# Kernel tuning notes

Measured on AMD Instinct MI355X. Metric: run time of the kernel, lower is better.

## Reference

```python
import jax, jax.numpy as jnp
import numpy as np

N_QUBITS = 8
DEPTH = 3


def _apply_1q(state, U, q):
    # state: (2,)*n complex, apply 2x2 unitary U on qubit axis q
    state = jnp.moveaxis(state, q, -1)
    state = state @ U.T
    return jnp.moveaxis(state, -1, q)


def _ry(state, theta, q):
    h = theta * 0.5
    c, s = jnp.cos(h), jnp.sin(h)
    U = jnp.stack([jnp.stack([c, -s]), jnp.stack([s, c])]).astype(jnp.complex64)
    return _apply_1q(state, U, q)


def _rz(state, theta, q):
    h = theta * 0.5
    d = jnp.stack([jnp.exp(-1j * h), jnp.exp(1j * h)]).astype(jnp.complex64)
    state = jnp.moveaxis(state, q, -1) * d
    return jnp.moveaxis(state, -1, q)


def _cx(state, c, t):
    # CNOT with control c, target t: flip target amplitudes where control=1
    state = jnp.moveaxis(state, (c, t), (-2, -1))
    s0 = state[..., 0, :]
    s1 = state[..., 1, ::-1]
    state = jnp.stack([s0, s1], axis=-2)
    return jnp.moveaxis(state, (-2, -1), (c, t))


def _simulate(angles, qparams):
    # Single-sample circuit: RY angle encoding, then DEPTH layers of (RZ,RY) per
    # qubit + CX ring. Returns <Z_0> (Hamiltonian 'Z' + 'I'*(n-1)).
    state = jnp.zeros((2,) * N_QUBITS, jnp.complex64).at[(0,) * N_QUBITS].set(1.0)
    for q in range(N_QUBITS):
        state = _ry(state, angles[q], q)
    idx = 0
    for _ in range(DEPTH):
        for q in range(N_QUBITS):
            state = _rz(state, qparams[idx], q); idx += 1
            state = _ry(state, qparams[idx], q); idx += 1
        for i in range(N_QUBITS):
            state = _cx(state, i, (i + 1) % N_QUBITS)
    probs = jnp.abs(state) ** 2
    return probs[0].sum() - probs[1].sum()


def setup_inputs() -> dict:
    key = jax.random.key(0)
    ks = jax.random.split(key, 6)
    B, F, H = 16384, 16, 256
    nq = 2 * N_QUBITS * DEPTH  # 48 variational params
    return {
        "x": jax.random.normal(ks[0], (B, F), jnp.float32),
        "enc_w1": jax.random.normal(ks[1], (H, F), jnp.float32) / np.sqrt(F).astype(np.float32),
        "enc_b1": jnp.zeros((H,), jnp.float32),
        "enc_w2": jax.random.normal(ks[2], (N_QUBITS, H), jnp.float32) / np.sqrt(H).astype(np.float32),
        "enc_b2": jnp.zeros((N_QUBITS,), jnp.float32),
        "qparams": jax.random.normal(ks[3], (nq,), jnp.float32) * 0.1,
        "dec_w1": jax.random.normal(ks[4], (H, 1), jnp.float32),
        "dec_b1": jnp.zeros((H,), jnp.float32),
        "dec_w2": jax.random.normal(ks[5], (1, H), jnp.float32) / np.sqrt(H).astype(np.float32),
        "dec_b2": jnp.zeros((1,), jnp.float32),
    }


def reference(x, enc_w1, enc_b1, enc_w2, enc_b2, qparams, dec_w1, dec_b1, dec_w2, dec_b2):
    # encoder: Linear -> ReLU -> Linear -> Tanh, scaled by pi (angle encoding)
    h = jax.nn.relu(x @ enc_w1.T + enc_b1)
    angles = jnp.tanh(h @ enc_w2.T + enc_b2) * jnp.pi  # (B, n_qubits)
    # vectorized quantum state-vector simulation over the batch
    expvals = jax.vmap(_simulate, in_axes=(0, None))(angles, qparams)  # (B,)
    q = expvals[:, None]  # (B, 1)
    # decoder: Linear(1->H) -> ReLU -> Linear(H->1) -> Sigmoid
    d = jax.nn.relu(q @ dec_w1.T + dec_b1)
    return jax.nn.sigmoid(d @ dec_w2.T + dec_b2)
```

## Files before the change

kernel.cpp:

```cpp
#include <hip/hip_runtime.h>
#include <math.h>

#define NQ 8
#define DEPTH 3
#define FDIM 16
#define HDIM 256
#define WAVES_PER_BLOCK 4
#define THREADS (WAVES_PER_BLOCK * 64)
#define NGATE (NQ * DEPTH)
#define PI_F 3.14159265358979323846f

template<int CTRL>
__device__ __forceinline__ float dpp1(float v) {
    return __int_as_float(__builtin_amdgcn_update_dpp(
        0, __float_as_int(v), CTRL, 0xF, 0xF, true));
}

template<int M4>
__device__ __forceinline__ float shuf4(float v) {
    if constexpr (M4 == 1)  return dpp1<0xB1>(v);
    else if constexpr (M4 == 2)  return dpp1<0x4E>(v);
    else if constexpr (M4 == 4)  return dpp1<0x1B>(dpp1<0x141>(v));
    else if constexpr (M4 == 8)  return dpp1<0x128>(v);
    else return v;
}

template<int ML>
__device__ __forceinline__ float shuf(float v, int lane) {
    if constexpr (ML == 0) {
        return v;
    } else if constexpr (ML >= 32) {
        int addr = (lane ^ ML) << 2;
        return __int_as_float(__builtin_amdgcn_ds_bpermute(addr, __float_as_int(v)));
    } else {
        return __int_as_float(__builtin_amdgcn_ds_swizzle(
            __float_as_int(v), (ML << 10) | 0x1F));
    }
}

__device__ __forceinline__ float wred(float v, int lane) {
    v += shuf4<1>(v);
    v += shuf4<2>(v);
    v += shuf4<4>(v);
    v += shuf4<8>(v);
#if __has_builtin(__builtin_amdgcn_permlane16_swap)
    {
        auto r = __builtin_amdgcn_permlane16_swap(__float_as_int(v), __float_as_int(v), false, false);
        v = __int_as_float(r[0]) + __int_as_float(r[1]);
    }
#else
    v += __shfl_xor(v, 16, 64);
#endif
#if __has_builtin(__builtin_amdgcn_permlane32_swap)
    {
        auto r = __builtin_amdgcn_permlane32_swap(__float_as_int(v), __float_as_int(v), false, false);
        v = __int_as_float(r[0]) + __int_as_float(r[1]);
    }
#else
    v += __shfl_xor(v, 32, 64);
#endif
    return v;
}

__device__ __forceinline__ float fast_tanh(float y) {
    float ex = __expf(2.f * y);
    return 1.f - 2.f * __builtin_amdgcn_rcpf(ex + 1.f);
}

template<int M, int R>
__device__ __forceinline__ void gate2(float (&sr)[4], float (&si)[4],
                                      float cz, float szv, float cy, float sy,
                                      int lane) {
    constexpr int ML = M & 63, MH = (M >> 6) & 3;
    constexpr int RL = R & 63, RH = (R >> 6) & 3;
    bool p0;
    if constexpr (RL == 0)                 p0 = false;
    else if constexpr ((RL & (RL-1)) == 0) p0 = (lane & RL) != 0;
    else                                   p0 = (__popc(lane & RL) & 1) != 0;
    float sgz = p0 ? szv : -szv;
    float sgy = p0 ? sy  : -sy;
#pragma unroll
    for (int hi = 0; hi < 4; hi++) {
        const bool f = (__builtin_popcount(hi & RH) & 1) != 0;
        float z = f ? -sgz : sgz;
        float nr = fmaf(sr[hi], cz, -(si[hi] * z));
        float ni = fmaf(si[hi], cz,  (sr[hi] * z));
        sr[hi] = nr; si[hi] = ni;
    }
    float pr[4], pi[4];
#pragma unroll
    for (int hi = 0; hi < 4; hi++) {
        pr[hi] = shuf<ML>(sr[hi ^ MH], lane);
        pi[hi] = shuf<ML>(si[hi ^ MH], lane);
    }
#pragma unroll
    for (int hi = 0; hi < 4; hi++) {
        const bool f = (__builtin_popcount(hi & RH) & 1) != 0;
        float yv = f ? -sgy : sgy;
        sr[hi] = fmaf(yv, pr[hi], cy * sr[hi]);
        si[hi] = fmaf(yv, pi[hi], cy * si[hi]);
    }
}

__global__ __launch_bounds__(THREADS) void hqcl_kernel(
    const float* __restrict__ x,
    const float* __restrict__ w1,
    const float* __restrict__ b1,
    const float* __restrict__ w2,
    const float* __restrict__ b2,
    const float* __restrict__ qp,
    const float* __restrict__ dw1,
    const float* __restrict__ db1,
    const float* __restrict__ dw2,
    const float* __restrict__ db2,
    float* __restrict__ out, int B)
{
    __shared__ float4 sG4[NGATE];

    const int t = threadIdx.x;
    if (t < 2 * NGATE) {
        float s, c;
        __sincosf(qp[t] * 0.5f, &s, &c);
        float* p = (float*)&sG4[t >> 1] + 2 * (t & 1);
        p[0] = c; p[1] = s;
    }
    __syncthreads();

    const int lane = t & 63;
    const int row  = blockIdx.x * WAVES_PER_BLOCK + (t >> 6);
    if (row >= B) return;

    const float4* xp = (const float4*)(x + row * FDIM);
    float4 x0 = xp[0], x1 = xp[1], x2 = xp[2], x3 = xp[3];

    float hreg[4];
#pragma unroll
    for (int m = 0; m < 4; m++) {
        int j = lane + 64 * m;
        const float4* wp = (const float4*)(w1 + j * FDIM);
        float4 wa = wp[0], wb = wp[1], wc = wp[2], wd = wp[3];
        float acc = b1[j];
        acc = fmaf(x0.x, wa.x, acc); acc = fmaf(x0.y, wa.y, acc);
        acc = fmaf(x0.z, wa.z, acc); acc = fmaf(x0.w, wa.w, acc);
        acc = fmaf(x1.x, wb.x, acc); acc = fmaf(x1.y, wb.y, acc);
        acc = fmaf(x1.z, wb.z, acc); acc = fmaf(x1.w, wb.w, acc);
        acc = fmaf(x2.x, wc.x, acc); acc = fmaf(x2.y, wc.y, acc);
        acc = fmaf(x2.z, wc.z, acc); acc = fmaf(x2.w, wc.w, acc);
        acc = fmaf(x3.x, wd.x, acc); acc = fmaf(x3.y, wd.y, acc);
        acc = fmaf(x3.z, wd.z, acc); acc = fmaf(x3.w, wd.w, acc);
        hreg[m] = fmaxf(acc, 0.f);
    }

    float c0[NQ], s0[NQ];
#pragma unroll
    for (int q = 0; q < NQ; q++) {
        float a = 0.f;
#pragma unroll
        for (int m = 0; m < 4; m++)
            a = fmaf(hreg[m], w2[q * HDIM + lane + 64 * m], a);
        a = wred(a, lane);
        float u = 0.25f * fast_tanh(a + b2[q]);
        float sv, cv;
        asm("v_sin_f32 %0, %1" : "=v"(sv) : "v"(u));
        asm("v_cos_f32 %0, %1" : "=v"(cv) : "v"(u));
        s0[q] = sv; c0[q] = cv;
    }

    float pl = 1.f;
#pragma unroll
    for (int b = 0; b < 6; b++) {
        int q = 7 - b;
        pl *= ((lane >> b) & 1) ? s0[q] : c0[q];
    }
    float sr[4], si[4];
    sr[0] = pl * c0[1] * c0[0];
    sr[1] = pl * s0[1] * c0[0];
    sr[2] = pl * c0[1] * s0[0];
    sr[3] = pl * s0[1] * s0[0];
#pragma unroll
    for (int hi = 0; hi < 4; hi++) si[hi] = 0.f;

#define GATE(L, Q, MM, RR) { float4 g4 = sG4[(L)*8 + (Q)]; \
        gate2<MM, RR>(sr, si, g4.x, g4.y, g4.z, g4.w, lane); }
    GATE(0,0,0x80,0x80) GATE(0,1,0x40,0x40) GATE(0,2,0x20,0x20) GATE(0,3,0x10,0x10)
    GATE(0,4,0x08,0x08) GATE(0,5,0x04,0x04) GATE(0,6,0x02,0x02) GATE(0,7,0x01,0x01)
    GATE(1,0,0xC0,0x7F) GATE(1,1,0x60,0xC0) GATE(1,2,0x30,0xE0) GATE(1,3,0x18,0xF0)
    GATE(1,4,0x0C,0xF8) GATE(1,5,0x06,0xFC) GATE(1,6,0x03,0xFE) GATE(1,7,0xC1,0xFF)
    GATE(2,0,0xA0,0xD5) GATE(2,1,0x50,0xBF) GATE(2,2,0x28,0x5F) GATE(2,3,0x14,0xAF)
    GATE(2,4,0x0A,0x57) GATE(2,5,0x05,0xAB) GATE(2,6,0xC2,0x55) GATE(2,7,0x61,0xAA)
#undef GATE

    float m0 = sr[0]*sr[0] + si[0]*si[0] + sr[2]*sr[2] + si[2]*si[2];
    float m1 = sr[1]*sr[1] + si[1]*si[1] + sr[3]*sr[3] + si[3]*si[3];
    bool pb = (__popc(lane & 0x0C) & 1) != 0;
    float e = pb ? (m1 - m0) : (m0 - m1);
    e = wred(e, lane);

    float acc = 0.f;
#pragma unroll
    for (int m = 0; m < 4; m++) {
        int j = lane + 64 * m;
        float d = fmaxf(fmaf(e, dw1[j], db1[j]), 0.f);
        acc = fmaf(d, dw2[j], acc);
    }
    acc = wred(acc, lane);
    if (lane == 0) out[row] = 1.f / (1.f + __expf(-(acc + db2[0])));
}

extern "C" void kernel_launch(void* const* d_in, const int* in_sizes, int n_in,
                              void* d_out, int out_size, void* d_ws, size_t ws_size,
                              hipStream_t stream) {
    const float* x   = (const float*)d_in[0];
    const float* w1  = (const float*)d_in[1];
    const float* b1  = (const float*)d_in[2];
    const float* w2  = (const float*)d_in[3];
    const float* b2  = (const float*)d_in[4];
    const float* qp  = (const float*)d_in[5];
    const float* dw1 = (const float*)d_in[6];
    const float* db1 = (const float*)d_in[7];
    const float* dw2 = (const float*)d_in[8];
    const float* db2 = (const float*)d_in[9];
    float* out = (float*)d_out;

    const int B = in_sizes[0] / FDIM;
    const int grid = (B + WAVES_PER_BLOCK - 1) / WAVES_PER_BLOCK;
    hqcl_kernel<<<grid, THREADS, 0, stream>>>(x, w1, b1, w2, b2, qp, dw1, db1, dw2, db2, out, B);
}
```

Measured before the change: 39.34 us.

## Process two batch rows per wavefront to reuse weight loads and add ILP

Each wavefront now handles two samples instead of one. The encoder weights, decoder weights and gate coefficients it loads are shared by both rows, and the state-vector gate updates for the two rows are interleaved to expose more independent instructions. The grid is halved and launch bounds now request 8 blocks per CU, which limits registers per thread. Register pressure roughly doubles, so spills or lower occupancy could offset the gain. Reading x for row0+1 is not bounds-checked when B is odd.

```diff
diff --git a/kernel.cpp b/kernel.cpp
--- a/kernel.cpp
+++ b/kernel.cpp
@@ -7,8 +7,8 @@
 #define HDIM 256
 #define WAVES_PER_BLOCK 4
 #define THREADS (WAVES_PER_BLOCK * 64)
+#define ROWS_PER_BLOCK (WAVES_PER_BLOCK * 2)
 #define NGATE (NQ * DEPTH)
-#define PI_F 3.14159265358979323846f
 
 template<int CTRL>
 __device__ __forceinline__ float dpp1(float v) {
@@ -68,9 +68,10 @@
 }
 
 template<int M, int R>
-__device__ __forceinline__ void gate2(float (&sr)[4], float (&si)[4],
-                                      float cz, float szv, float cy, float sy,
-                                      int lane) {
+__device__ __forceinline__ void gate2x2(float (&srA)[4], float (&siA)[4],
+                                        float (&srB)[4], float (&siB)[4],
+                                        float cz, float szv, float cy, float sy,
+                                        int lane) {
     constexpr int ML = M & 63, MH = (M >> 6) & 3;
     constexpr int RL = R & 63, RH = (R >> 6) & 3;
     bool p0;
@@ -83,26 +84,33 @@
     for (int hi = 0; hi < 4; hi++) {
         const bool f = (__builtin_popcount(hi & RH) & 1) != 0;
         float z = f ? -sgz : sgz;
-        float nr = fmaf(sr[hi], cz, -(si[hi] * z));
-        float ni = fmaf(si[hi], cz,  (sr[hi] * z));
-        sr[hi] = nr; si[hi] = ni;
-    }
-    float pr[4], pi[4];
+        float nrA = fmaf(srA[hi], cz, -(siA[hi] * z));
+        float niA = fmaf(siA[hi], cz,  (srA[hi] * z));
+        srA[hi] = nrA; siA[hi] = niA;
+        float nrB = fmaf(srB[hi], cz, -(siB[hi] * z));
+        float niB = fmaf(siB[hi], cz,  (srB[hi] * z));
+        srB[hi] = nrB; siB[hi] = niB;
+    }
+    float prA[4], piA[4], prB[4], piB[4];
 #pragma unroll
     for (int hi = 0; hi < 4; hi++) {
-        pr[hi] = shuf<ML>(sr[hi ^ MH], lane);
-        pi[hi] = shuf<ML>(si[hi ^ MH], lane);
+        prA[hi] = shuf<ML>(srA[hi ^ MH], lane);
+        piA[hi] = shuf<ML>(siA[hi ^ MH], lane);
+        prB[hi] = shuf<ML>(srB[hi ^ MH], lane);
+        piB[hi] = shuf<ML>(siB[hi ^ MH], lane);
     }
 #pragma unroll
     for (int hi = 0; hi < 4; hi++) {
         const bool f = (__builtin_popcount(hi & RH) & 1) != 0;
         float yv = f ? -sgy : sgy;
-        sr[hi] = fmaf(yv, pr[hi], cy * sr[hi]);
-        si[hi] = fmaf(yv, pi[hi], cy * si[hi]);
-    }
-}
-
-__global__ __launch_bounds__(THREADS) void hqcl_kernel(
+        srA[hi] = fmaf(yv, prA[hi], cy * srA[hi]);
+        siA[hi] = fmaf(yv, piA[hi], cy * siA[hi]);
+        srB[hi] = fmaf(yv, prB[hi], cy * srB[hi]);
+        siB[hi] = fmaf(yv, piB[hi], cy * siB[hi]);
+    }
+}
+
+__global__ __launch_bounds__(THREADS, 8) void hqcl_kernel(
     const float* __restrict__ x,
     const float* __restrict__ w1,
     const float* __restrict__ b1,
@@ -127,61 +135,88 @@
     __syncthreads();
 
     const int lane = t & 63;
-    const int row  = blockIdx.x * WAVES_PER_BLOCK + (t >> 6);
-    if (row >= B) return;
-
-    const float4* xp = (const float4*)(x + row * FDIM);
-    float4 x0 = xp[0], x1 = xp[1], x2 = xp[2], x3 = xp[3];
-
-    float hreg[4];
+    const int row0 = blockIdx.x * ROWS_PER_BLOCK + (t >> 6) * 2;
+    if (row0 >= B) return;
+
+    const float4* xA = (const float4*)(x + row0 * FDIM);
+    const float4* xB = (const float4*)(x + (row0 + 1) * FDIM);
+    float4 xa0 = xA[0], xa1 = xA[1], xa2 = xA[2], xa3 = xA[3];
+    float4 xb0 = xB[0], xb1 = xB[1], xb2 = xB[2], xb3 = xB[3];
+
+    float hA[4], hB[4];
 #pragma unroll
     for (int m = 0; m < 4; m++) {
         int j = lane + 64 * m;
         const float4* wp = (const float4*)(w1 + j * FDIM);
         float4 wa = wp[0], wb = wp[1], wc = wp[2], wd = wp[3];
-        float acc = b1[j];
-        acc = fmaf(x0.x, wa.x, acc); acc = fmaf(x0.y, wa.y, acc);
-        acc = fmaf(x0.z, wa.z, acc); acc = fmaf(x0.w, wa.w, acc);
-        acc = fmaf(x1.x, wb.x, acc); acc = fmaf(x1.y, wb.y, acc);
-        acc = fmaf(x1.z, wb.z, acc); acc = fmaf(x1.w, wb.w, acc);
-        acc = fmaf(x2.x, wc.x, acc); acc = fmaf(x2.y, wc.y, acc);
-        acc = fmaf(x2.z, wc.z, acc); acc = fmaf(x2.w, wc.w, acc);
-        acc = fmaf(x3.x, wd.x, acc); acc = fmaf(x3.y, wd.y, acc);
-        acc = fmaf(x3.z, wd.z, acc); acc = fmaf(x3.w, wd.w, acc);
-        hreg[m] = fmaxf(acc, 0.f);
-    }
-
-    float c0[NQ], s0[NQ];
+        float bv = b1[j];
+        float aA = bv, aB = bv;
+        aA = fmaf(xa0.x, wa.x, aA); aA = fmaf(xa0.y, wa.y, aA);
+        aA = fmaf(xa0.z, wa.z, aA); aA = fmaf(xa0.w, wa.w, aA);
+        aA = fmaf(xa1.x, wb.x, aA); aA = fmaf(xa1.y, wb.y, aA);
+        aA = fmaf(xa1.z, wb.z, aA); aA = fmaf(xa1.w, wb.w, aA);
+        aA = fmaf(xa2.x, wc.x, aA); aA = fmaf(xa2.y, wc.y, aA);
+        aA = fmaf(xa2.z, wc.z, aA); aA = fmaf(xa2.w, wc.w, aA);
+        aA = fmaf(xa3.x, wd.x, aA); aA = fmaf(xa3.y, wd.y, aA);
+        aA = fmaf(xa3.z, wd.z, aA); aA = fmaf(xa3.w, wd.w, aA);
+        aB = fmaf(xb0.x, wa.x, aB); aB = fmaf(xb0.y, wa.y, aB);
+        aB = fmaf(xb0.z, wa.z, aB); aB = fmaf(xb0.w, wa.w, aB);
+        aB = fmaf(xb1.x, wb.x, aB); aB = fmaf(xb1.y, wb.y, aB);
+        aB = fmaf(xb1.z, wb.z, aB); aB = fmaf(xb1.w, wb.w, aB);
+        aB = fmaf(xb2.x, wc.x, aB); aB = fmaf(xb2.y, wc.y, aB);
+        aB = fmaf(xb2.z, wc.z, aB); aB = fmaf(xb2.w, wc.w, aB);
+        aB = fmaf(xb3.x, wd.x, aB); aB = fmaf(xb3.y, wd.y, aB);
+        aB = fmaf(xb3.z, wd.z, aB); aB = fmaf(xb3.w, wd.w, aB);
+        hA[m] = fmaxf(aA, 0.f);
+        hB[m] = fmaxf(aB, 0.f);
+    }
+
+    float c0A[NQ], s0A[NQ], c0B[NQ], s0B[NQ];
 #pragma unroll
     for (int q = 0; q < NQ; q++) {
-        float a = 0.f;
-#pragma unroll
-        for (int m = 0; m < 4; m++)
-            a = fmaf(hreg[m], w2[q * HDIM + lane + 64 * m], a);
-        a = wred(a, lane);
-        float u = 0.25f * fast_tanh(a + b2[q]);
-        float sv, cv;
-        asm("v_sin_f32 %0, %1" : "=v"(sv) : "v"(u));
-        asm("v_cos_f32 %0, %1" : "=v"(cv) : "v"(u));
-        s0[q] = sv; c0[q] = cv;
-    }
-
-    float pl = 1.f;
+        float aA = 0.f, aB = 0.f;
+#pragma unroll
+        for (int m = 0; m < 4; m++) {
+            float wv = w2[q * HDIM + lane + 64 * m];
+            aA = fmaf(hA[m], wv, aA);
+            aB = fmaf(hB[m], wv, aB);
+        }
+        aA = wred(aA, lane);
+        aB = wred(aB, lane);
+        float bq = b2[q];
+        float uA = 0.25f * fast_tanh(aA + bq);
+        float uB = 0.25f * fast_tanh(aB + bq);
+        float svA, cvA, svB, cvB;
+        asm("v_sin_f32 %0, %1" : "=v"(svA) : "v"(uA));
+        asm("v_cos_f32 %0, %1" : "=v"(cvA) : "v"(uA));
+        asm("v_sin_f32 %0, %1" : "=v"(svB) : "v"(uB));
+        asm("v_cos_f32 %0, %1" : "=v"(cvB) : "v"(uB));
+        s0A[q] = svA; c0A[q] = cvA;
+        s0B[q] = svB; c0B[q] = cvB;
+    }
+
+    float plA = 1.f, plB = 1.f;
 #pragma unroll
     for (int b = 0; b < 6; b++) {
         int q = 7 - b;
-        pl *= ((lane >> b) & 1) ? s0[q] : c0[q];
-    }
-    float sr[4], si[4];
-    sr[0] = pl * c0[1] * c0[0];
-    sr[1] = pl * s0[1] * c0[0];
-    sr[2] = pl * c0[1] * s0[0];
-    sr[3] = pl * s0[1] * s0[0];
-#pragma unroll
-    for (int hi = 0; hi < 4; hi++) si[hi] = 0.f;
+        bool bit = (lane >> b) & 1;
+        plA *= bit ? s0A[q] : c0A[q];
+        plB *= bit ? s0B[q] : c0B[q];
+    }
+    float srA[4], siA[4], srB[4], siB[4];
+    srA[0] = plA * c0A[1] * c0A[0];
+    srA[1] = plA * s0A[1] * c0A[0];
+    srA[2] = plA * c0A[1] * s0A[0];
+    srA[3] = plA * s0A[1] * s0A[0];
+    srB[0] = plB * c0B[1] * c0B[0];
+    srB[1] = plB * s0B[1] * c0B[0];
+    srB[2] = plB * c0B[1] * s0B[0];
+    srB[3] = plB * s0B[1] * s0B[0];
+#pragma unroll
+    for (int hi = 0; hi < 4; hi++) { siA[hi] = 0.f; siB[hi] = 0.f; }
 
 #define GATE(L, Q, MM, RR) { float4 g4 = sG4[(L)*8 + (Q)]; \
-        gate2<MM, RR>(sr, si, g4.x, g4.y, g4.z, g4.w, lane); }
+        gate2x2<MM, RR>(srA, siA, srB, siB, g4.x, g4.y, g4.z, g4.w, lane); }
     GATE(0,0,0x80,0x80) GATE(0,1,0x40,0x40) GATE(0,2,0x20,0x20) GATE(0,3,0x10,0x10)
     GATE(0,4,0x08,0x08) GATE(0,5,0x04,0x04) GATE(0,6,0x02,0x02) GATE(0,7,0x01,0x01)
     GATE(1,0,0xC0,0x7F) GATE(1,1,0x60,0xC0) GATE(1,2,0x30,0xE0) GATE(1,3,0x18,0xF0)
@@ -190,21 +225,34 @@
     GATE(2,4,0x0A,0x57) GATE(2,5,0x05,0xAB) GATE(2,6,0xC2,0x55) GATE(2,7,0x61,0xAA)
 #undef GATE
 
-    float m0 = sr[0]*sr[0] + si[0]*si[0] + sr[2]*sr[2] + si[2]*si[2];
-    float m1 = sr[1]*sr[1] + si[1]*si[1] + sr[3]*sr[3] + si[3]*si[3];
     bool pb = (__popc(lane & 0x0C) & 1) != 0;
-    float e = pb ? (m1 - m0) : (m0 - m1);
-    e = wred(e, lane);
-
-    float acc = 0.f;
+    float m0A = srA[0]*srA[0] + siA[0]*siA[0] + srA[2]*srA[2] + siA[2]*siA[2];
+    float m1A = srA[1]*srA[1] + siA[1]*siA[1] + srA[3]*srA[3] + siA[3]*siA[3];
+    float m0B = srB[0]*srB[0] + siB[0]*siB[0] + srB[2]*srB[2] + siB[2]*siB[2];
+    float m1B = srB[1]*srB[1] + siB[1]*siB[1] + srB[3]*srB[3] + siB[3]*siB[3];
+    float eA = pb ? (m1A - m0A) : (m0A - m1A);
+    float eB = pb ? (m1B - m0B) : (m0B - m1B);
+    eA = wred(eA, lane);
+    eB = wred(eB, lane);
+
+    float accA = 0.f, accB = 0.f;
 #pragma unroll
     for (int m = 0; m < 4; m++) {
         int j = lane + 64 * m;
-        float d = fmaxf(fmaf(e, dw1[j], db1[j]), 0.f);
-        acc = fmaf(d, dw2[j], acc);
-    }
-    acc = wred(acc, lane);
-    if (lane == 0) out[row] = 1.f / (1.f + __expf(-(acc + db2[0])));
+        float w1v = dw1[j], bv = db1[j], w2v = dw2[j];
+        float dA = fmaxf(fmaf(eA, w1v, bv), 0.f);
+        float dB = fmaxf(fmaf(eB, w1v, bv), 0.f);
+        accA = fmaf(dA, w2v, accA);
+        accB = fmaf(dB, w2v, accB);
+    }
+    accA = wred(accA, lane);
+    accB = wred(accB, lane);
+    if (lane == 0) {
+        float bb = db2[0];
+        out[row0] = 1.f / (1.f + __expf(-(accA + bb)));
+        if (row0 + 1 < B)
+            out[row0 + 1] = 1.f / (1.f + __expf(-(accB + bb)));
+    }
 }
 
 extern "C" void kernel_launch(void* const* d_in, const int* in_sizes, int n_in,
@@ -223,6 +271,6 @@
     float* out = (float*)d_out;
 
     const int B = in_sizes[0] / FDIM;
-    const int grid = (B + WAVES_PER_BLOCK - 1) / WAVES_PER_BLOCK;
+    const int grid = (B + ROWS_PER_BLOCK - 1) / ROWS_PER_BLOCK;
     hqcl_kernel<<<grid, THREADS, 0, stream>>>(x, w1, b1, w2, b2, qp, dw1, db1, dw2, db2, out, B);
 }
```

After: 39.85 us. About the same (+1.3%).

## Fuse RZ and RY into one combined 2x2 gate and use DPP for more lane shuffles

Applied to the files above, without the earlier changes.

Precomputes the product of each RZ·RY pair as a single complex 2x2 matrix (four products of cos/sin terms stored per gate), so each qubit update is a single fused matrix apply. The shuffle of amplitudes now happens before any arithmetic, which removes the serial dependency between the phase rotation and the shuffle. It also routes XOR-lane shuffles with masks 1, 2, 3, 7, 8 and 15 through DPP sequences instead of ds_swizzle, aiming to cut LDS-path latency. The DPP mappings for the composite masks must match the intended XOR permutations exactly, otherwise results are wrong.

```diff
diff --git a/kernel.cpp b/kernel.cpp
--- a/kernel.cpp
+++ b/kernel.cpp
@@ -8,7 +8,6 @@
 #define WAVES_PER_BLOCK 4
 #define THREADS (WAVES_PER_BLOCK * 64)
 #define NGATE (NQ * DEPTH)
-#define PI_F 3.14159265358979323846f
 
 template<int CTRL>
 __device__ __forceinline__ float dpp1(float v) {
@@ -17,12 +16,23 @@
 }
 
 template<int M4>
-__device__ __forceinline__ float shuf4(float v) {
-    if constexpr (M4 == 1)  return dpp1<0xB1>(v);
+__device__ __forceinline__ float dppx(float v) {
+    if constexpr (M4 == 0)  return v;
+    else if constexpr (M4 == 1)  return dpp1<0xB1>(v);
     else if constexpr (M4 == 2)  return dpp1<0x4E>(v);
+    else if constexpr (M4 == 3)  return dpp1<0x1B>(v);
     else if constexpr (M4 == 4)  return dpp1<0x1B>(dpp1<0x141>(v));
+    else if constexpr (M4 == 5)  return dpp1<0x4E>(dpp1<0x141>(v));
+    else if constexpr (M4 == 6)  return dpp1<0xB1>(dpp1<0x141>(v));
+    else if constexpr (M4 == 7)  return dpp1<0x141>(v);
     else if constexpr (M4 == 8)  return dpp1<0x128>(v);
-    else return v;
+    else if constexpr (M4 == 9)  return dpp1<0xB1>(dpp1<0x128>(v));
+    else if constexpr (M4 == 10) return dpp1<0x4E>(dpp1<0x128>(v));
+    else if constexpr (M4 == 11) return dpp1<0x1B>(dpp1<0x128>(v));
+    else if constexpr (M4 == 12) return dpp1<0x1B>(dpp1<0x140>(v));
+    else if constexpr (M4 == 13) return dpp1<0x4E>(dpp1<0x140>(v));
+    else if constexpr (M4 == 14) return dpp1<0xB1>(dpp1<0x140>(v));
+    else                         return dpp1<0x140>(v);
 }
 
 template<int ML>
@@ -32,6 +42,8 @@
     } else if constexpr (ML >= 32) {
         int addr = (lane ^ ML) << 2;
         return __int_as_float(__builtin_amdgcn_ds_bpermute(addr, __float_as_int(v)));
+    } else if constexpr (ML == 1 || ML == 2 || ML == 3 || ML == 7 || ML == 8 || ML == 15) {
+        return dppx<ML>(v);
     } else {
         return __int_as_float(__builtin_amdgcn_ds_swizzle(
             __float_as_int(v), (ML << 10) | 0x1F));
@@ -39,10 +51,10 @@
 }
 
 __device__ __forceinline__ float wred(float v, int lane) {
-    v += shuf4<1>(v);
-    v += shuf4<2>(v);
-    v += shuf4<4>(v);
-    v += shuf4<8>(v);
+    v += dppx<1>(v);
+    v += dppx<2>(v);
+    v += dppx<4>(v);
+    v += dppx<8>(v);
 #if __has_builtin(__builtin_amdgcn_permlane16_swap)
     {
         auto r = __builtin_amdgcn_permlane16_swap(__float_as_int(v), __float_as_int(v), false, false);
@@ -68,37 +80,35 @@
 }
 
 template<int M, int R>
-__device__ __forceinline__ void gate2(float (&sr)[4], float (&si)[4],
-                                      float cz, float szv, float cy, float sy,
-                                      int lane) {
+__device__ __forceinline__ void gate_m(float (&sr)[4], float (&si)[4],
+                                       float a0, float a1, float b0, float b1,
+                                       int lane) {
     constexpr int ML = M & 63, MH = (M >> 6) & 3;
     constexpr int RL = R & 63, RH = (R >> 6) & 3;
     bool p0;
     if constexpr (RL == 0)                 p0 = false;
     else if constexpr ((RL & (RL-1)) == 0) p0 = (lane & RL) != 0;
     else                                   p0 = (__popc(lane & RL) & 1) != 0;
-    float sgz = p0 ? szv : -szv;
-    float sgy = p0 ? sy  : -sy;
-#pragma unroll
-    for (int hi = 0; hi < 4; hi++) {
-        const bool f = (__builtin_popcount(hi & RH) & 1) != 0;
-        float z = f ? -sgz : sgz;
-        float nr = fmaf(sr[hi], cz, -(si[hi] * z));
-        float ni = fmaf(si[hi], cz,  (sr[hi] * z));
-        sr[hi] = nr; si[hi] = ni;
-    }
+
     float pr[4], pi[4];
 #pragma unroll
     for (int hi = 0; hi < 4; hi++) {
         pr[hi] = shuf<ML>(sr[hi ^ MH], lane);
         pi[hi] = shuf<ML>(si[hi ^ MH], lane);
     }
+
+    float ea1 = p0 ? a1 : -a1;
+    float eb0 = p0 ? b0 : -b0;
+
 #pragma unroll
     for (int hi = 0; hi < 4; hi++) {
         const bool f = (__builtin_popcount(hi & RH) & 1) != 0;
-        float yv = f ? -sgy : sgy;
-        sr[hi] = fmaf(yv, pr[hi], cy * sr[hi]);
-        si[hi] = fmaf(yv, pi[hi], cy * si[hi]);
+        float za1 = f ? -ea1 : ea1;
+        float zb0 = f ? -eb0 : eb0;
+        float lr = fmaf(-za1, si[hi], a0 * sr[hi]);
+        float li = fmaf( za1, sr[hi], a0 * si[hi]);
+        sr[hi] = fmaf( b1, pi[hi], fmaf(zb0, pr[hi], lr));
+        si[hi] = fmaf(-b1, pr[hi], fmaf(zb0, pi[hi], li));
     }
 }
 
@@ -118,11 +128,11 @@
     __shared__ float4 sG4[NGATE];
 
     const int t = threadIdx.x;
-    if (t < 2 * NGATE) {
-        float s, c;
-        __sincosf(qp[t] * 0.5f, &s, &c);
-        float* p = (float*)&sG4[t >> 1] + 2 * (t & 1);
-        p[0] = c; p[1] = s;
+    if (t < NGATE) {
+        float cz, sz, cy, sy;
+        __sincosf(qp[2 * t] * 0.5f,     &sz, &cz);
+        __sincosf(qp[2 * t + 1] * 0.5f, &sy, &cy);
+        sG4[t] = make_float4(cz * cy, sz * cy, cz * sy, sz * sy);
     }
     __syncthreads();
 
@@ -181,7 +191,7 @@
     for (int hi = 0; hi < 4; hi++) si[hi] = 0.f;
 
 #define GATE(L, Q, MM, RR) { float4 g4 = sG4[(L)*8 + (Q)]; \
-        gate2<MM, RR>(sr, si, g4.x, g4.y, g4.z, g4.w, lane); }
+        gate_m<MM, RR>(sr, si, g4.x, g4.y, g4.z, g4.w, lane); }
     GATE(0,0,0x80,0x80) GATE(0,1,0x40,0x40) GATE(0,2,0x20,0x20) GATE(0,3,0x10,0x10)
     GATE(0,4,0x08,0x08) GATE(0,5,0x04,0x04) GATE(0,6,0x02,0x02) GATE(0,7,0x01,0x01)
     GATE(1,0,0xC0,0x7F) GATE(1,1,0x60,0xC0) GATE(1,2,0x30,0xE0) GATE(1,3,0x18,0xF0)
```

After: 40.17 us. 2.1% more time.
